# Performance work log

Hardware: AMD Instinct MI355X
Metric: run time of the kernel (lower is better)

## Reference

```python
import jax, jax.numpy as jnp
import numpy as np

# AF2 IPA dims
N, CS, CZ, E, PQ, PV, H = 768, 384, 128, 16, 4, 8, 12
SCALE_SINGLE = 1.0 / np.sqrt(E)
SCALE_FRAME = -1.0 / np.sqrt(18.0 * PQ)


def setup_inputs() -> dict:
    key = jax.random.key(0)
    ks = jax.random.split(key, 14)
    single = jax.random.normal(ks[0], (N, CS), jnp.float32)
    pair = jax.random.normal(ks[1], (N, N, CZ), jnp.float32)
    R, _ = jnp.linalg.qr(jax.random.normal(ks[2], (N, 3, 3), jnp.float32))  # proper per-residue rotations
    t = jax.random.normal(ks[3], (N, 3), jnp.float32)

    def w(k, shape):
        return jax.random.normal(k, shape, jnp.float32) / np.sqrt(shape[0])

    Wq = w(ks[4], (CS, H * E))
    Wk = w(ks[5], (CS, H * E))
    Wv = w(ks[6], (CS, H * E))
    Wqp = w(ks[7], (CS, H * PQ * 3))
    Wkp = w(ks[8], (CS, H * PQ * 3))
    Wvp = w(ks[9], (CS, H * PV * 3))
    Wb = w(ks[10], (CZ, H))
    D_out = H * (CZ + E + PV * 4)  # 2112
    Wout = w(ks[11], (D_out, CS))
    bout = jnp.zeros((CS,), jnp.float32)
    scale_head = jnp.ones((H,), jnp.float32)
    return dict(single_representation=single, pair_representation=pair,
                frame_rotations=R, frame_translations=t,
                Wq=Wq, Wk=Wk, Wv=Wv, Wqp=Wqp, Wkp=Wkp, Wvp=Wvp,
                Wb=Wb, Wout=Wout, bout=bout, scale_head=scale_head)


def reference(single_representation, pair_representation, frame_rotations, frame_translations,
              Wq, Wk, Wv, Wqp, Wkp, Wvp, Wb, Wout, bout, scale_head):
    s, z, R, t = single_representation, pair_representation, frame_rotations, frame_translations
    # --- attention weights from three sources ---
    q = (s @ Wq).reshape(N, H, E)
    k = (s @ Wk).reshape(N, H, E)
    v = (s @ Wv).reshape(N, H, E)
    w_single = SCALE_SINGLE * jnp.einsum('ihe,jhe->hij', q, k)  # [H,N,N]
    w_pair = (z @ Wb).transpose(2, 0, 1)                        # [H,N,N]

    qp = (s @ Wqp).reshape(N, H, PQ, 3)
    kp = (s @ Wkp).reshape(N, H, PQ, 3)
    # Frame.apply: x_global = R_n x + t_n
    gq = jnp.einsum('nab,nhpb->nhpa', R, qp) + t[:, None, None, :]
    gk = jnp.einsum('nab,nhpb->nhpa', R, kp) + t[:, None, None, :]
    # sum_p ||gq_i^hp - gk_j^hp||^2 expanded to avoid [N,N,H,P,3] intermediate
    sq_q = jnp.sum(gq * gq, axis=(-1, -2)).T   # [H,N]
    sq_k = jnp.sum(gk * gk, axis=(-1, -2)).T   # [H,N]
    dot = jnp.einsum('ihpc,jhpc->hij', gq, gk)
    d2 = sq_q[:, :, None] + sq_k[:, None, :] - 2.0 * dot  # [H,N,N]
    w_frame = SCALE_FRAME * jax.nn.softplus(scale_head)[:, None, None] * d2

    a = jax.nn.softmax(w_single + w_pair + w_frame, axis=-1)  # [H,N,N]

    # --- three value paths ---
    o_s = jnp.einsum('hij,jhe->ihe', a, v).reshape(N, H * E)
    o_z = jnp.einsum('hij,ijc->ihc', a, z).reshape(N, H * CZ)

    vp = (s @ Wvp).reshape(N, H, PV, 3)
    gv = jnp.einsum('nab,nhpb->nhpa', R, vp) + t[:, None, None, :]
    so = jnp.einsum('hij,jhpc->ihpc', a, gv)                    # [N,H,PV,3] in global frame
    # Frame.inverse applied: R_i^T (x - t_i)
    local = jnp.einsum('nba,nhpb->nhpa', R, so - t[:, None, None, :])
    pts = local.transpose(0, 2, 1, 3).reshape(N, PV * H * 3)    # (point, head, xyz) flatten
    norms = jnp.linalg.norm(local, axis=-1).transpose(0, 2, 1).reshape(N, PV * H)

    att = jnp.concatenate([o_s, o_z, pts, norms], axis=-1)      # [N, H*(E+CZ+4*PV)]
    return att @ Wout + bout
```

## Files before the change

### kernel.cpp

```cpp
#include <hip/hip_runtime.h>
#include <hip/hip_bf16.h>

#define NN 768
#define CSD 384
#define CZD 128
#define HD 12
#define DOUT 2112
#define II 2

#define SCALE_SINGLE 0.25f
#define SCALE_FRAME (-0.11785113019775793f)

#define OFF_WQ   0
#define OFF_WK   73728
#define OFF_WV   147456
#define OFF_WQP  221184
#define OFF_WKP  276480
#define OFF_WVP  331776
#define OFF_WOUT 442368
#define NBF_TOTAL 1253376

__device__ __forceinline__ float dot4f(float4 a, float4 b){
    return fmaf(a.x,b.x, fmaf(a.y,b.y, fmaf(a.z,b.z, a.w*b.w)));
}
__device__ __forceinline__ unsigned short f2bf(float f){
    unsigned u = __float_as_uint(f);
    return (unsigned short)((u + 0x7fffu + ((u >> 16) & 1u)) >> 16);
}
__device__ __forceinline__ float bf2f(unsigned short u){
    return __uint_as_float(((unsigned)u) << 16);
}

__global__ __launch_bounds__(256) void k_conv(
    const float* __restrict__ Wq, const float* __restrict__ Wk, const float* __restrict__ Wv,
    const float* __restrict__ Wqp, const float* __restrict__ Wkp, const float* __restrict__ Wvp,
    const float* __restrict__ Wout, unsigned short* __restrict__ dst)
{
    int idx = blockIdx.x*256 + threadIdx.x;
    if (idx >= NBF_TOTAL) return;
    const float* src; int off = idx;
    if (idx < OFF_WK)        { src = Wq;  }
    else if (idx < OFF_WV)   { src = Wk;  off -= OFF_WK;  }
    else if (idx < OFF_WQP)  { src = Wv;  off -= OFF_WV;  }
    else if (idx < OFF_WKP)  { src = Wqp; off -= OFF_WQP; }
    else if (idx < OFF_WVP)  { src = Wkp; off -= OFF_WKP; }
    else if (idx < OFF_WOUT) { src = Wvp; off -= OFF_WVP; }
    else                     { src = Wout; off -= OFF_WOUT; }
    dst[idx] = f2bf(src[off]);
}

__global__ __launch_bounds__(384) void k_proj(
    const float* __restrict__ s, const float* __restrict__ R, const float* __restrict__ tv,
    const unsigned short* __restrict__ wbf,
    float* __restrict__ q, float* __restrict__ k, float* __restrict__ v,
    float* __restrict__ gq, float* __restrict__ gk, float* __restrict__ gv,
    float* __restrict__ sqq, float* __restrict__ sqk)
{
    __shared__ float s_l[II*CSD];
    __shared__ float praw[II][576];
    __shared__ float sq_pt[II][96];
    int i0 = blockIdx.x * II, t = threadIdx.x;
    if (t < II*CSD/4){
        const float4* s4 = (const float4*)(s + (size_t)i0*CSD);
        ((float4*)s_l)[t] = s4[t];
    }
    __syncthreads();

    int cols[3] = {t, t+384, t+768};
    const unsigned short* Wp[3]; int st[3], lc[3];
    #pragma unroll
    for (int m=0;m<3;m++){
        int c = cols[m];
        if (c < 192){ Wp[m]=wbf+OFF_WQ;  st[m]=192; lc[m]=c; }
        else if (c < 384){ Wp[m]=wbf+OFF_WK;  st[m]=192; lc[m]=c-192; }
        else if (c < 576){ Wp[m]=wbf+OFF_WV;  st[m]=192; lc[m]=c-384; }
        else if (c < 720){ Wp[m]=wbf+OFF_WQP; st[m]=144; lc[m]=c-576; }
        else if (c < 864){ Wp[m]=wbf+OFF_WKP; st[m]=144; lc[m]=c-720; }
        else { Wp[m]=wbf+OFF_WVP; st[m]=288; lc[m]=c-864; }
    }
    float acc[3][II];
    #pragma unroll
    for (int m=0;m<3;m++)
        #pragma unroll
        for (int ii=0;ii<II;ii++) acc[m][ii]=0.f;

    #pragma unroll 4
    for (int r=0;r<CSD;r++){
        float w0 = bf2f(Wp[0][(size_t)r*st[0]+lc[0]]);
        float w1 = bf2f(Wp[1][(size_t)r*st[1]+lc[1]]);
        float w2 = bf2f(Wp[2][(size_t)r*st[2]+lc[2]]);
        #pragma unroll
        for (int ii=0;ii<II;ii++){
            float sv = s_l[ii*CSD + r];
            acc[0][ii] = fmaf(sv, w0, acc[0][ii]);
            acc[1][ii] = fmaf(sv, w1, acc[1][ii]);
            acc[2][ii] = fmaf(sv, w2, acc[2][ii]);
        }
    }
    #pragma unroll
    for (int m=0;m<3;m++){
        int c = cols[m];
        #pragma unroll
        for (int ii=0;ii<II;ii++){
            float val = acc[m][ii];
            size_t i = i0 + ii;
            if (c < 192) q[i*192 + c] = val;
            else if (c < 384) k[i*192 + (c-192)] = val;
            else if (c < 576) v[i*192 + (c-384)] = val;
            else praw[ii][c-576] = val;
        }
    }
    __syncthreads();

    if (t < 192){
        #pragma unroll
        for (int ii=0;ii<II;ii++){
            size_t i = i0 + ii;
            const float* Ri = R + i*9;
            float R00=Ri[0],R01=Ri[1],R02=Ri[2];
            float R10=Ri[3],R11=Ri[4],R12=Ri[5];
            float R20=Ri[6],R21=Ri[7],R22=Ri[8];
            float t0=tv[i*3+0],t1=tv[i*3+1],t2=tv[i*3+2];
            int src; float* dst; int sqslot=-1;
            if (t < 48){ src = t*3; dst = gq + i*144 + t*3; sqslot = t; }
            else if (t < 96){ int u=t-48; src = 144+u*3; dst = gk + i*144 + u*3; sqslot = 48+u; }
            else { int u=t-96; src = 288+u*3; dst = gv + i*288 + u*3; }
            float x=praw[ii][src], y=praw[ii][src+1], zc=praw[ii][src+2];
            float g0 = fmaf(R00,x, fmaf(R01,y, fmaf(R02,zc, t0)));
            float g1 = fmaf(R10,x, fmaf(R11,y, fmaf(R12,zc, t1)));
            float g2 = fmaf(R20,x, fmaf(R21,y, fmaf(R22,zc, t2)));
            dst[0]=g0; dst[1]=g1; dst[2]=g2;
            if (sqslot >= 0) sq_pt[ii][sqslot] = g0*g0 + g1*g1 + g2*g2;
        }
    }
    __syncthreads();
    if (t < II*HD){
        int ii = t / HD, h = t % HD;
        float s1 = sq_pt[ii][h*4]+sq_pt[ii][h*4+1]+sq_pt[ii][h*4+2]+sq_pt[ii][h*4+3];
        float s2 = sq_pt[ii][48+h*4]+sq_pt[ii][48+h*4+1]+sq_pt[ii][48+h*4+2]+sq_pt[ii][48+h*4+3];
        sqq[(size_t)(i0+ii)*HD + h] = s1;
        sqk[(size_t)(i0+ii)*HD + h] = s2;
    }
}

__global__ __launch_bounds__(512) void k_ipa(
    const float* __restrict__ z, const float* __restrict__ Wb, const float* __restrict__ scale_head,
    const float* __restrict__ q, const float* __restrict__ k,
    const float* __restrict__ gq, const float* __restrict__ gk,
    const float* __restrict__ sqq, const float* __restrict__ sqk,
    const float* __restrict__ v, const float* __restrict__ gv,
    const float* __restrict__ R, const float* __restrict__ tv,
    float* __restrict__ att)
{
    __shared__ float ztile[2][64][CZD];
    __shared__ float wbT[HD*CZD];
    __shared__ float qloc[360];
    __shared__ float a_l[HD][NN];
    __shared__ float so_l[288];

    int i = blockIdx.x, t = threadIdx.x;
    int wave = t >> 6, lane = t & 63;

    for (int idx=t; idx<HD*CZD; idx+=512){
        int h = idx >> 7, c = idx & 127;
        wbT[idx] = Wb[(size_t)c*HD + h];
    }
    if (t < 192) qloc[t] = q[(size_t)i*192 + t];
    else if (t < 336) qloc[t] = gq[(size_t)i*144 + (t-192)];
    else if (t < 348) qloc[t] = sqq[(size_t)i*HD + (t-336)];
    else if (t < 360){
        int h = t-348;
        float shv = scale_head[h];
        float sp = (shv > 20.f) ? shv : log1pf(__expf(shv));
        qloc[t] = SCALE_FRAME * sp;
    }

    const char* zi = (const char*)(z + (size_t)i*NN*CZD);
    float* zbase = &ztile[0][0][0];

#define STAGEL(JT, BUF) do { \
    const char* _zb = zi + (size_t)(JT)*32768; \
    char* _lb = (char*)zbase + (size_t)(BUF)*32768; \
    _Pragma("unroll") \
    for (int _m=0;_m<4;_m++){ \
        int _d = t*16 + _m*8192; \
        int _j = _d >> 9; \
        int _b = _d & 511; \
        int _sb = _b ^ ((_j & 31) << 4); \
        __builtin_amdgcn_global_load_lds((const __attribute__((address_space(1))) void*)(_zb + (size_t)_j*512 + _sb), \
            (__attribute__((address_space(3))) void*)(_lb + _d), 16, 0, 0); \
    } \
  } while(0)

#define STAGEB(JT, BUF) do { \
    const float* _s = (const float*)zi + (size_t)(JT)*4096 + t*4; \
    float* _d = zbase + (size_t)(BUF)*4096 + t*4; \
    __builtin_amdgcn_global_load_lds((const __attribute__((address_space(1))) void*)_s, \
        (__attribute__((address_space(3))) void*)_d, 16, 0, 0); \
    __builtin_amdgcn_global_load_lds((const __attribute__((address_space(1))) void*)(_s+2048), \
        (__attribute__((address_space(3))) void*)(_d+2048), 16, 0, 0); \
  } while(0)

    STAGEL(0, 0);

    int hg = (wave < 4) ? wave : (wave - 4);
    int h0 = hg * 3;
    float L[12][3];

    __syncthreads();

    {
        const float4* wb4 = (const float4*)wbT;
        const float4* qv4 = (const float4*)qloc;
        const float4* gq4 = (const float4*)(qloc + 192);
        int xoff = (lane & 31) << 4;

        for (int jt=0; jt<12; ++jt){
            int cur = jt & 1;
            if (jt+1 < 12) STAGEL(jt+1, cur^1);
            if (wave < 4){
                const char* zb = (const char*)(zbase + (size_t)cur*8192) + lane*512;
                float p0=0.f, p1=0.f, p2=0.f;
                #pragma unroll 8
                for (int c4=0; c4<32; ++c4){
                    float4 zv = *(const float4*)(zb + ((c4*16) ^ xoff));
                    p0 += dot4f(zv, wb4[(h0+0)*32 + c4]);
                    p1 += dot4f(zv, wb4[(h0+1)*32 + c4]);
                    p2 += dot4f(zv, wb4[(h0+2)*32 + c4]);
                }
                L[jt][0]=p0; L[jt][1]=p1; L[jt][2]=p2;
            } else {
                int jg = jt*64 + lane;
                const float4* kp  = (const float4*)(k  + (size_t)jg*192);
                const float4* gkp = (const float4*)(gk + (size_t)jg*144);
                #pragma unroll
                for (int hs=0; hs<3; ++hs){
                    int h = h0 + hs;
                    float sng = dot4f(qv4[h*4+0], kp[h*4+0]) + dot4f(qv4[h*4+1], kp[h*4+1])
                              + dot4f(qv4[h*4+2], kp[h*4+2]) + dot4f(qv4[h*4+3], kp[h*4+3]);
                    float fdot = dot4f(gq4[h*3+0], gkp[h*3+0]) + dot4f(gq4[h*3+1], gkp[h*3+1])
                               + dot4f(gq4[h*3+2], gkp[h*3+2]);
                    float d2 = qloc[336+h] + sqk[(size_t)jg*HD + h] - 2.0f*fdot;
                    L[jt][hs] = fmaf(SCALE_SINGLE, sng, qloc[348+h]*d2);
                }
            }
            __syncthreads();
        }
    }

    float* S_l = zbase;
    if (wave >= 4){
        int base = (hg*64 + lane) * 37;
        #pragma unroll
        for (int jt=0; jt<12; ++jt)
            #pragma unroll
            for (int hs=0; hs<3; ++hs)
                S_l[base + jt*3 + hs] = L[jt][hs];
    }
    __syncthreads();
    if (wave < 4){
        int base = (hg*64 + lane) * 37;
        #pragma unroll
        for (int jt=0; jt<12; ++jt)
            #pragma unroll
            for (int hs=0; hs<3; ++hs)
                L[jt][hs] += S_l[base + jt*3 + hs];

        #pragma unroll
        for (int hs=0; hs<3; ++hs){
            float m = -1e30f;
            #pragma unroll
            for (int jt=0; jt<12; ++jt) m = fmaxf(m, L[jt][hs]);
            #pragma unroll
            for (int off=32; off; off>>=1) m = fmaxf(m, __shfl_xor(m, off));
            float ssum = 0.f;
            #pragma unroll
            for (int jt=0; jt<12; ++jt){ float e = __expf(L[jt][hs]-m); L[jt][hs]=e; ssum += e; }
            #pragma unroll
            for (int off=32; off; off>>=1) ssum += __shfl_xor(ssum, off);
            float inv = 1.0f/ssum;
            #pragma unroll
            for (int jt=0; jt<12; ++jt){
                a_l[h0+hs][jt*64 + lane] = L[jt][hs]*inv;
            }
        }
    }
    __syncthreads();

    STAGEB(0, 0);

    int hs = 0;
    const float4* gsrc = nullptr;
    int gstride = 0;
    if (t < 384){ hs = t>>5; }
    else if (t < 432){ int u=t-384; hs = u>>2; gsrc = (const float4*)v  + hs*4 + (u&3); gstride = 48; }
    else if (t < 504){ int u=t-432; hs = u/6;  gsrc = (const float4*)gv + hs*6 + (u%6); gstride = 72; }
    float4 acc = {0.f,0.f,0.f,0.f};
    int c4 = t & 31;

    __syncthreads();

    for (int jt=0; jt<24; ++jt){
        int cur = jt & 1;
        if (jt+1 < 24) STAGEB(jt+1, cur^1);
        if (t < 384){
            const float4* arow4 = (const float4*)&a_l[hs][0];
            float4 af[8];
            #pragma unroll
            for (int m=0;m<8;m++) af[m] = arow4[jt*8 + m];
            const float4* zt4 = (const float4*)(zbase + (size_t)cur*4096);
            #pragma unroll
            for (int jj=0;jj<32;jj++){
                float aw = ((const float*)af)[jj];
                float4 zv = zt4[jj*32 + c4];
                acc.x = fmaf(aw, zv.x, acc.x);
                acc.y = fmaf(aw, zv.y, acc.y);
                acc.z = fmaf(aw, zv.z, acc.z);
                acc.w = fmaf(aw, zv.w, acc.w);
            }
        } else if (t < 504){
            const float* arow = &a_l[hs][0];
            #pragma unroll
            for (int jj=0;jj<32;jj++){
                int j = jt*32 + jj;
                float aw = arow[j];
                float4 sv = gsrc[(size_t)j*gstride];
                acc.x = fmaf(aw, sv.x, acc.x);
                acc.y = fmaf(aw, sv.y, acc.y);
                acc.z = fmaf(aw, sv.z, acc.z);
                acc.w = fmaf(aw, sv.w, acc.w);
            }
        }
        __syncthreads();
    }

    if (t < 384){
        float4* dst = (float4*)(att + (size_t)i*DOUT + 192) + (hs*32 + c4);
        *dst = acc;
    } else if (t < 432){
        int u = t-384;
        float4* dst = (float4*)(att + (size_t)i*DOUT) + u;
        *dst = acc;
    } else if (t < 504){
        int u = t-432;
        ((float4*)so_l)[u] = acc;
    }
    __syncthreads();
    if (t < 96){
        int h = t >> 3, p = t & 7;
        float d0 = so_l[h*24+p*3+0] - tv[(size_t)i*3+0];
        float d1 = so_l[h*24+p*3+1] - tv[(size_t)i*3+1];
        float d2 = so_l[h*24+p*3+2] - tv[(size_t)i*3+2];
        const float* Ri = R + (size_t)i*9;
        float l0 = fmaf(Ri[0],d0, fmaf(Ri[3],d1, Ri[6]*d2));
        float l1 = fmaf(Ri[1],d0, fmaf(Ri[4],d1, Ri[7]*d2));
        float l2 = fmaf(Ri[2],d0, fmaf(Ri[5],d1, Ri[8]*d2));
        size_t base = (size_t)i*DOUT;
        att[base + 1728 + p*36 + h*3 + 0] = l0;
        att[base + 1728 + p*36 + h*3 + 1] = l1;
        att[base + 1728 + p*36 + h*3 + 2] = l2;
        att[base + 2016 + p*12 + h] = sqrtf(l0*l0 + l1*l1 + l2*l2);
    }
#undef STAGEL
#undef STAGEB
}

#define ROWS4 2
__global__ __launch_bounds__(384) void k_final(
    const float* __restrict__ att, const unsigned short* __restrict__ wobf,
    const float* __restrict__ bout, float* __restrict__ out)
{
    __shared__ float att_l[ROWS4*DOUT];
    int ib = blockIdx.x * ROWS4, t = threadIdx.x;
    for (int idx=t; idx<ROWS4*DOUT; idx+=384){
        att_l[idx] = att[(size_t)ib*DOUT + idx];
    }
    __syncthreads();
    float a0=0.f,a1=0.f,a2=0.f,a3=0.f;
    float b0=0.f,b1=0.f,b2=0.f,b3=0.f;
    #pragma unroll 4
    for (int d=0; d<DOUT; d+=4){
        float w0 = bf2f(wobf[(size_t)(d+0)*CSD + t]);
        float w1 = bf2f(wobf[(size_t)(d+1)*CSD + t]);
        float w2 = bf2f(wobf[(size_t)(d+2)*CSD + t]);
        float w3 = bf2f(wobf[(size_t)(d+3)*CSD + t]);
        a0 = fmaf(att_l[d+0], w0, a0);
        a1 = fmaf(att_l[d+1], w1, a1);
        a2 = fmaf(att_l[d+2], w2, a2);
        a3 = fmaf(att_l[d+3], w3, a3);
        b0 = fmaf(att_l[DOUT+d+0], w0, b0);
        b1 = fmaf(att_l[DOUT+d+1], w1, b1);
        b2 = fmaf(att_l[DOUT+d+2], w2, b2);
        b3 = fmaf(att_l[DOUT+d+3], w3, b3);
    }
    float bb = bout[t];
    out[(size_t)ib*CSD + t]     = bb + ((a0+a1)+(a2+a3));
    out[(size_t)(ib+1)*CSD + t] = bb + ((b0+b1)+(b2+b3));
}

extern "C" void kernel_launch(void* const* d_in, const int* in_sizes, int n_in,
                              void* d_out, int out_size, void* d_ws, size_t ws_size,
                              hipStream_t stream)
{
    const float* s   = (const float*)d_in[0];
    const float* z   = (const float*)d_in[1];
    const float* R   = (const float*)d_in[2];
    const float* tv  = (const float*)d_in[3];
    const float* Wq  = (const float*)d_in[4];
    const float* Wk  = (const float*)d_in[5];
    const float* Wv  = (const float*)d_in[6];
    const float* Wqp = (const float*)d_in[7];
    const float* Wkp = (const float*)d_in[8];
    const float* Wvp = (const float*)d_in[9];
    const float* Wb  = (const float*)d_in[10];
    const float* Wout= (const float*)d_in[11];
    const float* bout= (const float*)d_in[12];
    const float* sh  = (const float*)d_in[13];

    float* ws  = (float*)d_ws;
    float* q_  = ws;
    float* k_  = q_  + 147456;
    float* v_  = k_  + 147456;
    float* gq_ = v_  + 147456;
    float* gk_ = gq_ + 110592;
    float* gv_ = gk_ + 110592;
    float* sqq_= gv_ + 221184;
    float* sqk_= sqq_ + 9216;
    float* att_= sqk_ + 9216;
    unsigned short* wbf = (unsigned short*)(att_ + 1622016);
    float* out = (float*)d_out;

    hipLaunchKernelGGL(k_conv,  dim3((NBF_TOTAL+255)/256), dim3(256), 0, stream,
                       Wq,Wk,Wv,Wqp,Wkp,Wvp,Wout, wbf);
    hipLaunchKernelGGL(k_proj,  dim3(NN/II), dim3(384), 0, stream,
                       s,R,tv, wbf, q_,k_,v_,gq_,gk_,gv_,sqq_,sqk_);
    hipLaunchKernelGGL(k_ipa,   dim3(NN),    dim3(512), 0, stream,
                       z,Wb,sh,q_,k_,gq_,gk_,sqq_,sqk_, v_,gv_,R,tv, att_);
    hipLaunchKernelGGL(k_final, dim3(NN/ROWS4), dim3(384), 0, stream,
                       att_, wbf + OFF_WOUT, bout, out);
}
```

Before: 391.0 us.

## Double k_ipa block to 1024 threads, one wave per head in both phases

```diff
diff --git a/kernel.cpp b/kernel.cpp
--- a/kernel.cpp
+++ b/kernel.cpp
@@ -143,7 +143,7 @@
     }
 }
 
-__global__ __launch_bounds__(512) void k_ipa(
+__global__ __launch_bounds__(1024) void k_ipa(
     const float* __restrict__ z, const float* __restrict__ Wb, const float* __restrict__ scale_head,
     const float* __restrict__ q, const float* __restrict__ k,
     const float* __restrict__ gq, const float* __restrict__ gk,
@@ -161,7 +161,7 @@
     int i = blockIdx.x, t = threadIdx.x;
     int wave = t >> 6, lane = t & 63;
 
-    for (int idx=t; idx<HD*CZD; idx+=512){
+    for (int idx=t; idx<HD*CZD; idx+=1024){
         int h = idx >> 7, c = idx & 127;
         wbT[idx] = Wb[(size_t)c*HD + h];
     }
@@ -182,8 +182,8 @@
     const char* _zb = zi + (size_t)(JT)*32768; \
     char* _lb = (char*)zbase + (size_t)(BUF)*32768; \
     _Pragma("unroll") \
-    for (int _m=0;_m<4;_m++){ \
-        int _d = t*16 + _m*8192; \
+    for (int _m=0;_m<2;_m++){ \
+        int _d = t*16 + _m*16384; \
         int _j = _d >> 9; \
         int _b = _d & 511; \
         int _sb = _b ^ ((_j & 31) << 4); \
@@ -193,18 +193,19 @@
   } while(0)
 
 #define STAGEB(JT, BUF) do { \
-    const float* _s = (const float*)zi + (size_t)(JT)*4096 + t*4; \
-    float* _d = zbase + (size_t)(BUF)*4096 + t*4; \
-    __builtin_amdgcn_global_load_lds((const __attribute__((address_space(1))) void*)_s, \
-        (__attribute__((address_space(3))) void*)_d, 16, 0, 0); \
-    __builtin_amdgcn_global_load_lds((const __attribute__((address_space(1))) void*)(_s+2048), \
-        (__attribute__((address_space(3))) void*)(_d+2048), 16, 0, 0); \
+    const char* _zb = zi + (size_t)(JT)*32768; \
+    char* _lb = (char*)zbase + (size_t)(BUF)*32768; \
+    _Pragma("unroll") \
+    for (int _m=0;_m<2;_m++){ \
+        int _d = t*16 + _m*16384; \
+        __builtin_amdgcn_global_load_lds((const __attribute__((address_space(1))) void*)(_zb + _d), \
+            (__attribute__((address_space(3))) void*)(_lb + _d), 16, 0, 0); \
+    } \
   } while(0)
 
     STAGEL(0, 0);
 
-    int hg = (wave < 4) ? wave : (wave - 4);
-    int h0 = hg * 3;
+    int gS = wave - 12;
     float L[12][3];
 
     __syncthreads();
@@ -218,24 +219,22 @@
         for (int jt=0; jt<12; ++jt){
             int cur = jt & 1;
             if (jt+1 < 12) STAGEL(jt+1, cur^1);
-            if (wave < 4){
+            if (wave < 12){
                 const char* zb = (const char*)(zbase + (size_t)cur*8192) + lane*512;
-                float p0=0.f, p1=0.f, p2=0.f;
+                float p0=0.f;
                 #pragma unroll 8
                 for (int c4=0; c4<32; ++c4){
                     float4 zv = *(const float4*)(zb + ((c4*16) ^ xoff));
-                    p0 += dot4f(zv, wb4[(h0+0)*32 + c4]);
-                    p1 += dot4f(zv, wb4[(h0+1)*32 + c4]);
-                    p2 += dot4f(zv, wb4[(h0+2)*32 + c4]);
+                    p0 += dot4f(zv, wb4[wave*32 + c4]);
                 }
-                L[jt][0]=p0; L[jt][1]=p1; L[jt][2]=p2;
+                L[jt][0]=p0;
             } else {
                 int jg = jt*64 + lane;
                 const float4* kp  = (const float4*)(k  + (size_t)jg*192);
                 const float4* gkp = (const float4*)(gk + (size_t)jg*144);
                 #pragma unroll
                 for (int hs=0; hs<3; ++hs){
-                    int h = h0 + hs;
+                    int h = gS*3 + hs;
                     float sng = dot4f(qv4[h*4+0], kp[h*4+0]) + dot4f(qv4[h*4+1], kp[h*4+1])
                               + dot4f(qv4[h*4+2], kp[h*4+2]) + dot4f(qv4[h*4+3], kp[h*4+3]);
                     float fdot = dot4f(gq4[h*3+0], gkp[h*3+0]) + dot4f(gq4[h*3+1], gkp[h*3+1])
@@ -249,8 +248,8 @@
     }
 
     float* S_l = zbase;
-    if (wave >= 4){
-        int base = (hg*64 + lane) * 37;
+    if (wave >= 12){
+        int base = (gS*64 + lane) * 37;
         #pragma unroll
         for (int jt=0; jt<12; ++jt)
             #pragma unroll
@@ -258,92 +257,89 @@
                 S_l[base + jt*3 + hs] = L[jt][hs];
     }
     __syncthreads();
-    if (wave < 4){
-        int base = (hg*64 + lane) * 37;
+    if (wave < 12){
+        int h = wave;
+        int base = ((h/3)*64 + lane) * 37;
+        int hs = h % 3;
         #pragma unroll
         for (int jt=0; jt<12; ++jt)
-            #pragma unroll
-            for (int hs=0; hs<3; ++hs)
-                L[jt][hs] += S_l[base + jt*3 + hs];
-
-        #pragma unroll
-        for (int hs=0; hs<3; ++hs){
-            float m = -1e30f;
-            #pragma unroll
-            for (int jt=0; jt<12; ++jt) m = fmaxf(m, L[jt][hs]);
-            #pragma unroll
-            for (int off=32; off; off>>=1) m = fmaxf(m, __shfl_xor(m, off));
-            float ssum = 0.f;
-            #pragma unroll
-            for (int jt=0; jt<12; ++jt){ float e = __expf(L[jt][hs]-m); L[jt][hs]=e; ssum += e; }
-            #pragma unroll
-            for (int off=32; off; off>>=1) ssum += __shfl_xor(ssum, off);
-            float inv = 1.0f/ssum;
-            #pragma unroll
-            for (int jt=0; jt<12; ++jt){
-                a_l[h0+hs][jt*64 + lane] = L[jt][hs]*inv;
-            }
-        }
+            L[jt][0] += S_l[base + jt*3 + hs];
+
+        float m = -1e30f;
+        #pragma unroll
+        for (int jt=0; jt<12; ++jt) m = fmaxf(m, L[jt][0]);
+        #pragma unroll
+        for (int off=32; off; off>>=1) m = fmaxf(m, __shfl_xor(m, off));
+        float ssum = 0.f;
+        #pragma unroll
+        for (int jt=0; jt<12; ++jt){ float e = __expf(L[jt][0]-m); L[jt][0]=e; ssum += e; }
+        #pragma unroll
+        for (int off=32; off; off>>=1) ssum += __shfl_xor(ssum, off);
+        float inv = 1.0f/ssum;
+        #pragma unroll
+        for (int jt=0; jt<12; ++jt)
+            a_l[h][jt*64 + lane] = L[jt][0]*inv;
     }
     __syncthreads();
 
     STAGEB(0, 0);
 
-    int hs = 0;
-    const float4* gsrc = nullptr;
-    int gstride = 0;
-    if (t < 384){ hs = t>>5; }
-    else if (t < 432){ int u=t-384; hs = u>>2; gsrc = (const float4*)v  + hs*4 + (u&3); gstride = 48; }
-    else if (t < 504){ int u=t-432; hs = u/6;  gsrc = (const float4*)gv + hs*6 + (u%6); gstride = 72; }
-    float4 acc = {0.f,0.f,0.f,0.f};
-    int c4 = t & 31;
-
-    __syncthreads();
-
-    for (int jt=0; jt<24; ++jt){
+    int c4 = lane & 31, jhalf = lane >> 5;
+    float4 az = {0,0,0,0};
+    float4 accs = {0,0,0,0};
+    const float4* gsrc = nullptr; int gstride = 0; int hso = 0;
+    if (t >= 768 && t < 816){ int u=t-768; hso = u>>2; gsrc = (const float4*)v  + hso*4 + (u&3); gstride = 48; }
+    else if (t >= 816 && t < 888){ int u=t-816; hso = u/6;  gsrc = (const float4*)gv + hso*6 + (u%6); gstride = 72; }
+
+    __syncthreads();
+
+    for (int jt=0; jt<12; ++jt){
         int cur = jt & 1;
-        if (jt+1 < 24) STAGEB(jt+1, cur^1);
-        if (t < 384){
-            const float4* arow4 = (const float4*)&a_l[hs][0];
+        if (jt+1 < 12) STAGEB(jt+1, cur^1);
+        if (wave < 12){
+            int h = wave;
+            const float4* arow4 = (const float4*)&a_l[h][0] + jt*16 + jhalf*8;
             float4 af[8];
             #pragma unroll
-            for (int m=0;m<8;m++) af[m] = arow4[jt*8 + m];
-            const float4* zt4 = (const float4*)(zbase + (size_t)cur*4096);
+            for (int m=0;m<8;m++) af[m] = arow4[m];
+            const float4* zt4 = (const float4*)(zbase + (size_t)cur*8192) + (size_t)jhalf*1024;
             #pragma unroll
             for (int jj=0;jj<32;jj++){
                 float aw = ((const float*)af)[jj];
                 float4 zv = zt4[jj*32 + c4];
-                acc.x = fmaf(aw, zv.x, acc.x);
-                acc.y = fmaf(aw, zv.y, acc.y);
-                acc.z = fmaf(aw, zv.z, acc.z);
-                acc.w = fmaf(aw, zv.w, acc.w);
+                az.x = fmaf(aw, zv.x, az.x);
+                az.y = fmaf(aw, zv.y, az.y);
+                az.z = fmaf(aw, zv.z, az.z);
+                az.w = fmaf(aw, zv.w, az.w);
             }
-        } else if (t < 504){
-            const float* arow = &a_l[hs][0];
+        } else if (t >= 768 && t < 888){
+            const float* arow = &a_l[hso][0];
             #pragma unroll
-            for (int jj=0;jj<32;jj++){
-                int j = jt*32 + jj;
+            for (int jj=0;jj<64;jj++){
+                int j = jt*64 + jj;
                 float aw = arow[j];
                 float4 sv = gsrc[(size_t)j*gstride];
-                acc.x = fmaf(aw, sv.x, acc.x);
-                acc.y = fmaf(aw, sv.y, acc.y);
-                acc.z = fmaf(aw, sv.z, acc.z);
-                acc.w = fmaf(aw, sv.w, acc.w);
+                accs.x = fmaf(aw, sv.x, accs.x);
+                accs.y = fmaf(aw, sv.y, accs.y);
+                accs.z = fmaf(aw, sv.z, accs.z);
+                accs.w = fmaf(aw, sv.w, accs.w);
             }
         }
         __syncthreads();
     }
 
-    if (t < 384){
-        float4* dst = (float4*)(att + (size_t)i*DOUT + 192) + (hs*32 + c4);
-        *dst = acc;
-    } else if (t < 432){
-        int u = t-384;
-        float4* dst = (float4*)(att + (size_t)i*DOUT) + u;
-        *dst = acc;
-    } else if (t < 504){
-        int u = t-432;
-        ((float4*)so_l)[u] = acc;
+    if (wave < 12){
+        az.x += __shfl_xor(az.x, 32); az.y += __shfl_xor(az.y, 32);
+        az.z += __shfl_xor(az.z, 32); az.w += __shfl_xor(az.w, 32);
+        if (jhalf == 0){
+            *(float4*)(att + (size_t)i*DOUT + 192 + wave*128 + c4*4) = az;
+        }
+    } else if (t >= 768 && t < 816){
+        int u = t-768;
+        ((float4*)(att + (size_t)i*DOUT))[u] = accs;
+    } else if (t >= 816 && t < 888){
+        int u = t-816;
+        ((float4*)so_l)[u] = accs;
     }
     __syncthreads();
     if (t < 96){
@@ -434,7 +430,7 @@
                        Wq,Wk,Wv,Wqp,Wkp,Wvp,Wout, wbf);
     hipLaunchKernelGGL(k_proj,  dim3(NN/II), dim3(384), 0, stream,
                        s,R,tv, wbf, q_,k_,v_,gq_,gk_,gv_,sqq_,sqk_);
-    hipLaunchKernelGGL(k_ipa,   dim3(NN),    dim3(512), 0, stream,
+    hipLaunchKernelGGL(k_ipa,   dim3(NN),    dim3(1024), 0, stream,
                        z,Wb,sh,q_,k_,gq_,gk_,sqq_,sqk_, v_,gv_,R,tv, att_);
     hipLaunchKernelGGL(k_final, dim3(NN/ROWS4), dim3(384), 0, stream,
                        att_, wbf + OFF_WOUT, bout, out);
```

After: 545.3 us. 39.5% more time.
